# Kernel tuning notes

Hardware: AMD Instinct MI355X
Metric: run time of the kernel (lower is better)

## Reference

```python
import jax, jax.numpy as jnp
import numpy as np

B, S, D_IN = 2, 2048, 1024
H, DA, DH = 16, 64, 64          # num_heads, attention_dim, head_dim (linear_hidden_dim)
EMBED = 1024
KSIZE = 1


def causal_conv1d(x_bsc, w):
    """x_bsc: (B,S,Cin); w: (Cout,Cin,K). Left-pad K-1 -> causal. Returns (B,Cout,S)."""
    k = w.shape[-1]
    x_bcs = jnp.transpose(x_bsc, (0, 2, 1))
    x_bcs = jnp.pad(x_bcs, ((0, 0), (0, 0), (k - 1, 0)))
    return jax.lax.conv_general_dilated(
        x_bcs, w, window_strides=(1,), padding='VALID',
        dimension_numbers=('NCH', 'OIH', 'NCH'))


def setup_inputs() -> dict:
    key = jax.random.key(0)
    ks = jax.random.split(key, 7)
    x = jax.random.normal(ks[0], (B, S, D_IN), dtype=jnp.float32)
    # causal mask: 1 where attended, 0 where masked (masked_fill where ==0)
    attn_mask = jnp.tril(jnp.ones((S, S), dtype=jnp.int32))[None, None]  # (1,1,S,S)
    wq = 0.02 * jax.random.normal(ks[1], (H * DA, D_IN, KSIZE), dtype=jnp.float32)
    wk = 0.02 * jax.random.normal(ks[2], (H * DA, D_IN, KSIZE), dtype=jnp.float32)
    wv = 0.02 * jax.random.normal(ks[3], (H * DH, D_IN, KSIZE), dtype=jnp.float32)
    w_out = 0.02 * jax.random.normal(ks[4], (EMBED, H * DH), dtype=jnp.float32)
    b_out = 0.02 * jax.random.normal(ks[5], (EMBED,), dtype=jnp.float32)
    return {"x": x, "attn_mask": attn_mask, "wq": wq, "wk": wk, "wv": wv,
            "w_out": w_out, "b_out": b_out}


def reference(x, attn_mask, wq, wk, wv, w_out, b_out):
    b, s, _ = x.shape
    scale = DH ** (-0.5)  # NOTE: torch code scales by head_dim, not attention_dim
    q = causal_conv1d(x, wq)  # (B, H*DA, S)
    k = causal_conv1d(x, wk)  # (B, H*DA, S)
    v = causal_conv1d(x, wv)  # (B, H*DH, S)
    q = q.reshape(b, H, DA, s).transpose(0, 1, 3, 2)  # (B,H,S,DA)
    k = k.reshape(b, H, DA, s).transpose(0, 1, 3, 2)
    v = v.reshape(b, H, DH, s).transpose(0, 1, 3, 2)  # (B,H,S,DH)
    scores = scale * jnp.einsum('bhnd,bhmd->bhnm', q, k)
    scores = jnp.where(attn_mask == 0, -jnp.inf, scores)
    probs = jax.nn.softmax(scores, axis=-1)
    context = jnp.einsum('bhnm,bhmd->bhnd', probs, v)  # (B,H,S,DH)
    context = context.transpose(0, 2, 1, 3).reshape(b, s, H * DH)
    return context @ w_out.T + b_out
```

## Files before the change

kernel.cpp:

```cpp
#include <hip/hip_runtime.h>
#include <math.h>


typedef __bf16 bf16;
typedef __bf16 bf16x8 __attribute__((ext_vector_type(8)));
typedef __bf16 bf16x4 __attribute__((ext_vector_type(4)));
typedef float  f32x4  __attribute__((ext_vector_type(4)));

#define MFMA16(a, b, c) __builtin_amdgcn_mfma_f32_16x16x32_bf16((a), (b), (c), 0, 0, 0)

__device__ __forceinline__ void gll16(const void* g, void* l) {
    __builtin_amdgcn_global_load_lds(
        (__attribute__((address_space(1))) unsigned int*)g,
        (__attribute__((address_space(3))) unsigned int*)l, 16, 0, 0);
}

__global__ __launch_bounds__(256) void cvt_all_kernel(
    const float* __restrict__ x,  const float* __restrict__ wq,
    const float* __restrict__ wk, const float* __restrict__ wv,
    const float* __restrict__ wo,
    bf16* __restrict__ xb,  bf16* __restrict__ wqb, bf16* __restrict__ wkb,
    bf16* __restrict__ wvb, bf16* __restrict__ wob)
{
    #pragma unroll
    for (int k = 0; k < 4; k++) {
        const int blk = blockIdx.x * 4 + k;
        const float* src; bf16* dst; int off; float scale = 1.f;
        if (blk < 4096)      { src = x;  dst = xb;  off = blk * 1024; }
        else if (blk < 5120) { src = wq; dst = wqb; off = (blk - 4096) * 1024;
                               scale = 0.18033688011112042f; }
        else if (blk < 6144) { src = wk; dst = wkb; off = (blk - 5120) * 1024; }
        else if (blk < 7168) { src = wv; dst = wvb; off = (blk - 6144) * 1024; }
        else                 { src = wo; dst = wob; off = (blk - 7168) * 1024; }
        const int i = off + threadIdx.x * 4;
        f32x4 v = *(const f32x4*)(src + i);
        bf16x4 o;
        o[0] = (bf16)(v[0] * scale); o[1] = (bf16)(v[1] * scale);
        o[2] = (bf16)(v[2] * scale); o[3] = (bf16)(v[3] * scale);
        *(bf16x4*)(dst + i) = o;
    }
}

__global__ __launch_bounds__(256, 3) void qkv_mfma_kernel(
    const bf16* __restrict__ xb, const bf16* __restrict__ wqb,
    const bf16* __restrict__ wkb, const bf16* __restrict__ wvb,
    bf16* __restrict__ Qb, bf16* __restrict__ Kb, bf16* __restrict__ Vtb)
{
    __shared__ bf16 As[2][128 * 32];
    __shared__ bf16 Bs[2][128 * 32];
    const int lin = blockIdx.x + 32 * blockIdx.y;
    const int xcd = lin & 7, lid = lin >> 3;
    const int rem = xcd * 96 + lid;
    const int mt = rem & 31;
    const int nt = rem >> 5;
    const int which = nt >> 3;
    const bf16* Wm = (which == 0) ? wqb : (which == 1) ? wkb : wvb;

    const int t = threadIdx.x;
    const int w = t >> 6, lane = t & 63, quad = lane >> 4, l16 = lane & 15;
    const int wm = (w >> 1) * 64, wn = (w & 1) * 64;
    const int srow = lane >> 2;
    const int scol = (lane & 3) * 8;

    const bf16* Ab = xb + ((size_t)(mt * 128) + srow) * 1024 + scol;
    const bf16* Bb = Wm + ((size_t)((nt & 7) * 128) + srow) * 1024 + scol;

    f32x4 acc[4][4];
    #pragma unroll
    for (int i = 0; i < 4; i++)
        #pragma unroll
        for (int j = 0; j < 4; j++)
            #pragma unroll
            for (int r = 0; r < 4; r++) acc[i][j][r] = 0.f;

    gll16(Ab + (size_t)(w * 16) * 1024,       As[0] + w * 512);
    gll16(Ab + (size_t)((w + 4) * 16) * 1024, As[0] + (w + 4) * 512);
    gll16(Bb + (size_t)(w * 16) * 1024,       Bs[0] + w * 512);
    gll16(Bb + (size_t)((w + 4) * 16) * 1024, Bs[0] + (w + 4) * 512);

    for (int it = 0; it < 32; it++) {
        const int cur = it & 1, nxt = cur ^ 1;
        __syncthreads();
        if (it < 31) {
            const int kn = it * 32 + 32;
            gll16(Ab + (size_t)(w * 16) * 1024 + kn,       As[nxt] + w * 512);
            gll16(Ab + (size_t)((w + 4) * 16) * 1024 + kn, As[nxt] + (w + 4) * 512);
            gll16(Bb + (size_t)(w * 16) * 1024 + kn,       Bs[nxt] + w * 512);
            gll16(Bb + (size_t)((w + 4) * 16) * 1024 + kn, Bs[nxt] + (w + 4) * 512);
        }
        bf16x8 af[4], bfr[4];
        #pragma unroll
        for (int i = 0; i < 4; i++)
            af[i] = *(const bf16x8*)&As[cur][(wm + i * 16 + l16) * 32 + quad * 8];
        #pragma unroll
        for (int j = 0; j < 4; j++)
            bfr[j] = *(const bf16x8*)&Bs[cur][(wn + j * 16 + l16) * 32 + quad * 8];
        #pragma unroll
        for (int i = 0; i < 4; i++)
            #pragma unroll
            for (int j = 0; j < 4; j++)
                acc[i][j] = MFMA16(af[i], bfr[j], acc[i][j]);
    }

    const int nbase = (nt & 7) * 128 + wn;
    if (which == 2) {
        #pragma unroll
        for (int i = 0; i < 4; i++) {
            const int m0 = mt * 128 + wm + i * 16 + quad * 4;
            const int bb = m0 >> 11, s0 = m0 & 2047;
            #pragma unroll
            for (int j = 0; j < 4; j++) {
                const int n = nbase + j * 16 + l16;
                const int h = n >> 6, d = n & 63;
                bf16x4 pk;
                #pragma unroll
                for (int r = 0; r < 4; r++) pk[r] = (bf16)acc[i][j][r];
                *(bf16x4*)&Vtb[(((size_t)(bb * 16 + h)) * 64 + d) * 2048 + s0] = pk;
            }
        }
    } else {
        bf16* Out = (which == 0) ? Qb : Kb;
        #pragma unroll
        for (int i = 0; i < 4; i++) {
            #pragma unroll
            for (int r = 0; r < 4; r++) {
                const int m = mt * 128 + wm + i * 16 + quad * 4 + r;
                const int bb = m >> 11, s = m & 2047;
                #pragma unroll
                for (int j = 0; j < 4; j++) {
                    const int n = nbase + j * 16 + l16;
                    const int h = n >> 6, d = n & 63;
                    Out[(((size_t)(bb * 16 + h)) * 2048 + s) * 64 + d] =
                        (bf16)acc[i][j][r];
                }
            }
        }
    }
}

__global__ __launch_bounds__(256, 2) void attn_mfma_kernel(
    const bf16* __restrict__ Qb, const bf16* __restrict__ Kb,
    const bf16* __restrict__ Vtb, bf16* __restrict__ ctxb)
{
    __shared__ bf16 Ks[2][128 * 64];
    __shared__ bf16 Vts[2][64 * 128];
    __shared__ bf16 Pl[4][16 * 128];

    const int id = blockIdx.x;
    const int bh = id & 31;
    const int pr = id >> 5;
    const int qa = pr, qb = 31 - pr;
    const int h = bh & 15, b = bh >> 4;
    const int t = threadIdx.x;
    const int w = t >> 6, lane = t & 63, quad = lane >> 4, l16 = lane & 15;

    const size_t hb = (size_t)(b * 16 + h);
    const bf16* Qh = Qb + hb * (2048 * 64);
    const bf16* Kh = Kb + hb * (2048 * 64);
    const bf16* Vh = Vtb + hb * (64 * 2048);

    bf16x8 qf0[2], qf1[2];
    {
        const bf16* Qr0 = Qh + (size_t)(qa * 64 + w * 16 + l16) * 64;
        qf0[0] = *(const bf16x8*)(Qr0 + quad * 8);
        qf0[1] = *(const bf16x8*)(Qr0 + 32 + quad * 8);
        const bf16* Qr1 = Qh + (size_t)(qb * 64 + w * 16 + l16) * 64;
        qf1[0] = *(const bf16x8*)(Qr1 + quad * 8);
        qf1[1] = *(const bf16x8*)(Qr1 + 32 + quad * 8);
    }

    bf16x8 ones;
    #pragma unroll
    for (int i = 0; i < 8; i++) ones[i] = (bf16)1.0f;

    f32x4 o0[4], o1[4], l0, l1;
    #pragma unroll
    for (int r = 0; r < 4; r++) { l0[r] = 0.f; l1[r] = 0.f; }
    #pragma unroll
    for (int dt = 0; dt < 4; dt++)
        #pragma unroll
        for (int r = 0; r < 4; r++) { o0[dt][r] = 0.f; o1[dt][r] = 0.f; }

    const int ksr = lane >> 3, ksc = lane & 7;
    const int vsr = lane >> 4, vsc = lane & 15;

    #define STAGE(ktv, buf)                                                   \
        {                                                                     \
            _Pragma("unroll")                                                 \
            for (int j = 0; j < 4; j++) {                                     \
                const int c = 4 * w + j;                                      \
                const int kr = c * 8 + ksr;                                   \
                gll16(Kh + (size_t)((ktv) * 128 + kr) * 64 +                  \
                          ((ksc ^ (kr & 7)) * 8),                             \
                      Ks[buf] + c * 512);                                     \
                const int vr = c * 4 + vsr;                                   \
                gll16(Vh + (size_t)vr * 2048 + (ktv) * 128 +                  \
                          ((vsc ^ (vr & 15)) * 8),                            \
                      Vts[buf] + c * 512);                                    \
            }                                                                 \
        }

    #define ITER(qt64, ktv, diag, qfv, oacc, lacc, cur)                       \
        {                                                                     \
            f32x4 sacc[8];                                                    \
            __builtin_amdgcn_s_setprio(1);                                    \
            _Pragma("unroll")                                                 \
            for (int tt = 0; tt < 8; tt++) {                                  \
                _Pragma("unroll")                                             \
                for (int r = 0; r < 4; r++) sacc[tt][r] = 0.f;                \
                const int krow = tt * 16 + l16;                               \
                bf16x8 kf0 = *(const bf16x8*)&Ks[cur][krow * 64 +             \
                                 ((quad)     ^ (krow & 7)) * 8];              \
                bf16x8 kf1 = *(const bf16x8*)&Ks[cur][krow * 64 +             \
                                 ((quad + 4) ^ (krow & 7)) * 8];              \
                sacc[tt] = MFMA16(kf0, (qfv)[0], sacc[tt]);                   \
                sacc[tt] = MFMA16(kf1, (qfv)[1], sacc[tt]);                   \
            }                                                                 \
            __builtin_amdgcn_s_setprio(0);                                    \
            const int qrow = (qt64) * 64 + w * 16 + l16;                      \
            _Pragma("unroll")                                                 \
            for (int tt = 0; tt < 8; tt++) {                                  \
                bf16x4 pk;                                                    \
                _Pragma("unroll")                                             \
                for (int r = 0; r < 4; r++) {                                 \
                    float p = __builtin_amdgcn_exp2f(sacc[tt][r]);            \
                    if ((diag) && ((ktv) * 128 + tt * 16 + quad * 4 + r) > qrow) \
                        p = 0.f;                                              \
                    pk[r] = (bf16)p;                                          \
                }                                                             \
                const int cs = (tt * 2 + (quad >> 1)) ^ l16;                  \
                *(bf16x4*)&Pl[w][l16 * 128 + cs * 8 + (quad & 1) * 4] = pk;   \
            }                                                                 \
            bf16x8 ap[4];                                                     \
            __builtin_amdgcn_s_setprio(1);                                    \
            _Pragma("unroll")                                                 \
            for (int u = 0; u < 4; u++) {                                     \
                ap[u] = *(const bf16x8*)&Pl[w][l16 * 128 +                    \
                             ((quad + 4 * u) ^ l16) * 8];                     \
                (lacc) = MFMA16(ap[u], ones, (lacc));                         \
            }                                                                 \
            _Pragma("unroll")                                                 \
            for (int dt = 0; dt < 4; dt++) {                                  \
                const int drow = dt * 16 + l16;                               \
                _Pragma("unroll")                                             \
                for (int u = 0; u < 4; u++) {                                 \
                    bf16x8 bv = *(const bf16x8*)&Vts[cur][drow * 128 +        \
                                     ((4 * u + quad) ^ (drow & 15)) * 8];     \
                    (oacc)[dt] = MFMA16(ap[u], bv, (oacc)[dt]);               \
                }                                                             \
            }                                                                 \
            __builtin_amdgcn_s_setprio(0);                                    \
        }

    const int na = (qa >> 1) + 1;
    STAGE(0, 0);

    for (int v = 0; v < 17; v++) {
        const int cur = v & 1, nxt = cur ^ 1;
        __syncthreads();
        if (v < 16) {
            const int vn = v + 1;
            const int ktn = (vn < na) ? vn : vn - na;
            STAGE(ktn, nxt);
        }
        if (v < na) {
            ITER(qa, v, (v == na - 1), qf0, o0, l0, cur);
        } else {
            const int kt = v - na;
            ITER(qb, kt, (v == 16), qf1, o1, l1, cur);
        }
    }
    #undef STAGE
    #undef ITER

    #pragma unroll
    for (int r = 0; r < 4; r++) {
        const float inv0 = 1.f / l0[r];
        const int s0 = qa * 64 + w * 16 + quad * 4 + r;
        const float inv1 = 1.f / l1[r];
        const int s1 = qb * 64 + w * 16 + quad * 4 + r;
        #pragma unroll
        for (int dt = 0; dt < 4; dt++) {
            ctxb[((size_t)(b * 2048 + s0)) * 1024 + h * 64 + dt * 16 + l16] =
                (bf16)(o0[dt][r] * inv0);
            ctxb[((size_t)(b * 2048 + s1)) * 1024 + h * 64 + dt * 16 + l16] =
                (bf16)(o1[dt][r] * inv1);
        }
    }
}

__global__ __launch_bounds__(256, 2) void oproj_mfma_kernel(
    const bf16* __restrict__ ctxb, const bf16* __restrict__ wob,
    const float* __restrict__ b_out, float* __restrict__ out)
{
    __shared__ bf16 As[2][64 * 32];
    __shared__ bf16 Bs[2][128 * 32];
    const int mt = blockIdx.x;
    const int nt = blockIdx.y;
    const int t = threadIdx.x;
    const int w = t >> 6, lane = t & 63, quad = lane >> 4, l16 = lane & 15;
    const int srow = lane >> 2;
    const int scol = (lane & 3) * 8;

    const bf16* Ab = ctxb + (size_t)(mt * 64 + srow) * 1024 + scol;
    const bf16* Bb = wob + (size_t)(nt * 128 + srow) * 1024 + scol;

    const int wrow = (w >> 1) * 32;
    const int wcol = (w & 1) * 64;

    f32x4 acc[2][4];
    #pragma unroll
    for (int i = 0; i < 2; i++)
        #pragma unroll
        for (int j = 0; j < 4; j++)
            #pragma unroll
            for (int r = 0; r < 4; r++) acc[i][j][r] = 0.f;

    gll16(Ab + (size_t)(w * 16) * 1024,       As[0] + w * 512);
    gll16(Bb + (size_t)(w * 16) * 1024,       Bs[0] + w * 512);
    gll16(Bb + (size_t)((w + 4) * 16) * 1024, Bs[0] + (w + 4) * 512);

    for (int it = 0; it < 32; it++) {
        const int cur = it & 1, nxt = cur ^ 1;
        __syncthreads();
        if (it < 31) {
            const int kn = it * 32 + 32;
            gll16(Ab + (size_t)(w * 16) * 1024 + kn,       As[nxt] + w * 512);
            gll16(Bb + (size_t)(w * 16) * 1024 + kn,       Bs[nxt] + w * 512);
            gll16(Bb + (size_t)((w + 4) * 16) * 1024 + kn, Bs[nxt] + (w + 4) * 512);
        }
        bf16x8 af0 = *(const bf16x8*)&As[cur][(wrow + l16) * 32 + quad * 8];
        bf16x8 af1 = *(const bf16x8*)&As[cur][(wrow + 16 + l16) * 32 + quad * 8];
        #pragma unroll
        for (int j = 0; j < 4; j++) {
            bf16x8 bv = *(const bf16x8*)&Bs[cur][(wcol + j * 16 + l16) * 32 + quad * 8];
            acc[0][j] = MFMA16(af0, bv, acc[0][j]);
            acc[1][j] = MFMA16(af1, bv, acc[1][j]);
        }
    }

    #pragma unroll
    for (int i = 0; i < 2; i++)
        #pragma unroll
        for (int j = 0; j < 4; j++)
            #pragma unroll
            for (int r = 0; r < 4; r++) {
                const int m = mt * 64 + wrow + i * 16 + quad * 4 + r;
                const int n = nt * 128 + wcol + j * 16 + l16;
                out[(size_t)m * 1024 + n] = acc[i][j][r] + b_out[n];
            }
}

extern "C" void kernel_launch(void* const* d_in, const int* in_sizes, int n_in,
                              void* d_out, int out_size, void* d_ws, size_t ws_size,
                              hipStream_t stream)
{
    const float* x     = (const float*)d_in[0];
    const float* wq    = (const float*)d_in[2];
    const float* wk    = (const float*)d_in[3];
    const float* wv    = (const float*)d_in[4];
    const float* w_out = (const float*)d_in[5];
    const float* b_out = (const float*)d_in[6];
    float* out = (float*)d_out;

    char* ws = (char*)d_ws;
    bf16* xb   = (bf16*)(ws);
    bf16* wqb  = (bf16*)(ws + (8u  << 20));
    bf16* wkb  = (bf16*)(ws + (10u << 20));
    bf16* wvb  = (bf16*)(ws + (12u << 20));
    bf16* wob  = (bf16*)(ws + (14u << 20));
    bf16* Qb   = (bf16*)(ws + (16u << 20));
    bf16* Kb   = (bf16*)(ws + (24u << 20));
    bf16* Vtb  = (bf16*)(ws + (32u << 20));
    bf16* ctxb = (bf16*)(ws + (40u << 20));

    cvt_all_kernel<<<2048, 256, 0, stream>>>(x, wq, wk, wv, w_out,
                                             xb, wqb, wkb, wvb, wob);
    qkv_mfma_kernel<<<dim3(32, 24), 256, 0, stream>>>(xb, wqb, wkb, wvb, Qb, Kb, Vtb);
    attn_mfma_kernel<<<512, 256, 0, stream>>>(Qb, Kb, Vtb, ctxb);
    oproj_mfma_kernel<<<dim3(64, 8), 256, 0, stream>>>(ctxb, wob, b_out, out);
}
```

Measured before the change: 187.1 us.

## Rewrite QKV projection GEMM with 256x256 tiles, 8 waves, swizzled LDS and fine-grained pipeline

Replaces the 128x128x32 double-buffered QKV GEMM with a 256x256 tile computed by 512-thread blocks (8 waves), using K-steps of 64 and XOR-swizzled LDS layouts to avoid bank conflicts. The main loop interleaves global-to-LDS loads of half-tiles with MFMA phases under explicit barriers, vmcnt waits and setprio, so loads overlap with compute. This raises arithmetic intensity and cuts global traffic per FLOP, but the grid shrinks to 192 blocks, which may underfill the device, and register and LDS pressure rise.

```diff
diff --git a/kernel.cpp b/kernel.cpp
--- a/kernel.cpp
+++ b/kernel.cpp
@@ -41,96 +41,187 @@
     }
 }
 
-__global__ __launch_bounds__(256, 3) void qkv_mfma_kernel(
+__global__ __launch_bounds__(512, 2) void qkv_mfma_kernel(
     const bf16* __restrict__ xb, const bf16* __restrict__ wqb,
     const bf16* __restrict__ wkb, const bf16* __restrict__ wvb,
     bf16* __restrict__ Qb, bf16* __restrict__ Kb, bf16* __restrict__ Vtb)
 {
-    __shared__ bf16 As[2][128 * 32];
-    __shared__ bf16 Bs[2][128 * 32];
-    const int lin = blockIdx.x + 32 * blockIdx.y;
-    const int xcd = lin & 7, lid = lin >> 3;
-    const int rem = xcd * 96 + lid;
-    const int mt = rem & 31;
-    const int nt = rem >> 5;
-    const int which = nt >> 3;
+    __shared__ bf16 Asm[2][2][128 * 64];
+    __shared__ bf16 Bsm[2][2][128 * 64];
+
+    const int lin = blockIdx.x;
+    const int rem = (lin & 7) * 24 + (lin >> 3);
+    const int mt = rem / 12;
+    const int nt = rem % 12;
+    const int which = nt >> 2;
     const bf16* Wm = (which == 0) ? wqb : (which == 1) ? wkb : wvb;
 
     const int t = threadIdx.x;
     const int w = t >> 6, lane = t & 63, quad = lane >> 4, l16 = lane & 15;
-    const int wm = (w >> 1) * 64, wn = (w & 1) * 64;
-    const int srow = lane >> 2;
-    const int scol = (lane & 3) * 8;
-
-    const bf16* Ab = xb + ((size_t)(mt * 128) + srow) * 1024 + scol;
-    const bf16* Bb = Wm + ((size_t)((nt & 7) * 128) + srow) * 1024 + scol;
-
-    f32x4 acc[4][4];
-    #pragma unroll
-    for (int i = 0; i < 4; i++)
+    const int ha  = w >> 2;
+    const int hbi = (w & 3) >> 1;
+    const int br0 = (w & 1) * 64;
+
+    const int srA = w * 8 + (lane >> 3);
+    const int scg = ((lane & 7) ^ (lane >> 3)) * 8;
+
+    const int MT0 = mt * 256;
+    const int NT0 = (nt & 3) * 256;
+
+    const int xr = l16 & 7;
+    const int cg0 = ((quad)     ^ xr) * 8;
+    const int cg1 = ((quad + 4) ^ xr) * 8;
+
+    f32x4 acc[8][4];
+    #pragma unroll
+    for (int i = 0; i < 8; i++)
         #pragma unroll
         for (int j = 0; j < 4; j++)
             #pragma unroll
             for (int r = 0; r < 4; r++) acc[i][j][r] = 0.f;
 
-    gll16(Ab + (size_t)(w * 16) * 1024,       As[0] + w * 512);
-    gll16(Ab + (size_t)((w + 4) * 16) * 1024, As[0] + (w + 4) * 512);
-    gll16(Bb + (size_t)(w * 16) * 1024,       Bs[0] + w * 512);
-    gll16(Bb + (size_t)((w + 4) * 16) * 1024, Bs[0] + (w + 4) * 512);
-
-    for (int it = 0; it < 32; it++) {
-        const int cur = it & 1, nxt = cur ^ 1;
-        __syncthreads();
-        if (it < 31) {
-            const int kn = it * 32 + 32;
-            gll16(Ab + (size_t)(w * 16) * 1024 + kn,       As[nxt] + w * 512);
-            gll16(Ab + (size_t)((w + 4) * 16) * 1024 + kn, As[nxt] + (w + 4) * 512);
-            gll16(Bb + (size_t)(w * 16) * 1024 + kn,       Bs[nxt] + w * 512);
-            gll16(Bb + (size_t)((w + 4) * 16) * 1024 + kn, Bs[nxt] + (w + 4) * 512);
-        }
-        bf16x8 af[4], bfr[4];
-        #pragma unroll
-        for (int i = 0; i < 4; i++)
-            af[i] = *(const bf16x8*)&As[cur][(wm + i * 16 + l16) * 32 + quad * 8];
-        #pragma unroll
-        for (int j = 0; j < 4; j++)
-            bfr[j] = *(const bf16x8*)&Bs[cur][(wn + j * 16 + l16) * 32 + quad * 8];
-        #pragma unroll
-        for (int i = 0; i < 4; i++)
-            #pragma unroll
-            for (int j = 0; j < 4; j++)
-                acc[i][j] = MFMA16(af[i], bfr[j], acc[i][j]);
-    }
-
-    const int nbase = (nt & 7) * 128 + wn;
+    bf16x8 af0[4][2], af1[4][2], bf0[2][2], bf1[2][2];
+
+#define STG(gb, R0, kb, dst)                                                  \
+    gll16((gb) + (size_t)((R0) + srA) * 1024 + (kb) + scg, (dst) + w * 512);  \
+    gll16((gb) + (size_t)((R0) + 64 + srA) * 1024 + (kb) + scg,               \
+          (dst) + 4096 + w * 512);
+
+#define LDA(dst, DB, IB)                                                      \
+    _Pragma("unroll")                                                         \
+    for (int ii = 0; ii < 4; ii++) {                                          \
+        const int ro = ((IB) + ii) * 16 + l16;                                \
+        dst[ii][0] = *(const bf16x8*)&Asm[DB][ha][ro * 64 + cg0];             \
+        dst[ii][1] = *(const bf16x8*)&Asm[DB][ha][ro * 64 + cg1];             \
+    }
+
+#define LDB(dst, DB, JB)                                                      \
+    _Pragma("unroll")                                                         \
+    for (int jj = 0; jj < 2; jj++) {                                          \
+        const int ro = br0 + ((JB) + jj) * 16 + l16;                          \
+        dst[jj][0] = *(const bf16x8*)&Bsm[DB][hbi][ro * 64 + cg0];            \
+        dst[jj][1] = *(const bf16x8*)&Bsm[DB][hbi][ro * 64 + cg1];            \
+    }
+
+#define MM(afv, IB, bfv, JB)                                                  \
+    __builtin_amdgcn_s_setprio(1);                                            \
+    _Pragma("unroll")                                                         \
+    for (int ii = 0; ii < 4; ii++)                                            \
+        _Pragma("unroll")                                                     \
+        for (int jj = 0; jj < 2; jj++) {                                      \
+            acc[(IB) + ii][(JB) + jj] =                                       \
+                MFMA16(afv[ii][0], bfv[jj][0], acc[(IB) + ii][(JB) + jj]);    \
+            acc[(IB) + ii][(JB) + jj] =                                       \
+                MFMA16(afv[ii][1], bfv[jj][1], acc[(IB) + ii][(JB) + jj]);    \
+        }                                                                     \
+    __builtin_amdgcn_s_setprio(0);
+
+#define BARR __builtin_amdgcn_s_barrier()
+#define LG0  asm volatile("s_waitcnt lgkmcnt(0)" ::: "memory")
+#define VM4  asm volatile("s_waitcnt vmcnt(4)" ::: "memory")
+#define VM0  asm volatile("s_waitcnt vmcnt(0)" ::: "memory")
+
+    STG(xb, MT0,       0, &Asm[0][0][0]);
+    STG(xb, MT0 + 128, 0, &Asm[0][1][0]);
+    STG(Wm, NT0,       0, &Bsm[0][0][0]);
+    STG(Wm, NT0 + 128, 0, &Bsm[0][1][0]);
+    STG(Wm, NT0,      64, &Bsm[1][0][0]);
+    STG(Wm, NT0 + 128,64, &Bsm[1][1][0]);
+    VM4;
+    BARR;
+
+    for (int tt = 0; tt < 8; tt++) {
+        const int kB = tt * 128 + 64;
+        const int kC = tt * 128 + 128;
+        const int kD = tt * 128 + 192;
+        const bool more = (tt < 7);
+
+        LDA(af0, 0, 0); LDB(bf0, 0, 0);
+        STG(xb, MT0,       kB, &Asm[1][0][0]);
+        BARR; LG0;
+        MM(af0, 0, bf0, 0);
+        BARR;
+
+        LDA(af1, 0, 4); LDB(bf1, 0, 2);
+        STG(xb, MT0 + 128, kB, &Asm[1][1][0]);
+        BARR; LG0;
+        MM(af1, 4, bf0, 0);
+        BARR;
+
+        if (more) { STG(Wm, NT0,       kC, &Bsm[0][0][0]); }
+        BARR;
+        MM(af0, 0, bf1, 2);
+        BARR;
+
+        if (more) { STG(Wm, NT0 + 128, kC, &Bsm[0][1][0]); }
+        BARR;
+        MM(af1, 4, bf1, 2);
+        if (more) { VM4; } else { VM0; }
+        BARR;
+
+        LDA(af0, 1, 0); LDB(bf0, 1, 0);
+        if (more) { STG(xb, MT0,       kC, &Asm[0][0][0]); }
+        BARR; LG0;
+        MM(af0, 0, bf0, 0);
+        BARR;
+
+        LDA(af1, 1, 4); LDB(bf1, 1, 2);
+        if (more) { STG(xb, MT0 + 128, kC, &Asm[0][1][0]); }
+        BARR; LG0;
+        MM(af1, 4, bf0, 0);
+        BARR;
+
+        if (more) { STG(Wm, NT0,       kD, &Bsm[1][0][0]); }
+        BARR;
+        MM(af0, 0, bf1, 2);
+        BARR;
+
+        if (more) { STG(Wm, NT0 + 128, kD, &Bsm[1][1][0]); }
+        BARR;
+        MM(af1, 4, bf1, 2);
+        VM4;
+        BARR;
+    }
+
+#undef STG
+#undef LDA
+#undef LDB
+#undef MM
+#undef BARR
+#undef LG0
+#undef VM4
+#undef VM0
+
+    const int wrowg = MT0 + ha * 128;
+    const int ncol  = NT0 + (w & 3) * 64;
     if (which == 2) {
         #pragma unroll
-        for (int i = 0; i < 4; i++) {
-            const int m0 = mt * 128 + wm + i * 16 + quad * 4;
+        for (int i = 0; i < 8; i++) {
+            const int m0 = wrowg + i * 16 + quad * 4;
             const int bb = m0 >> 11, s0 = m0 & 2047;
             #pragma unroll
             for (int j = 0; j < 4; j++) {
-                const int n = nbase + j * 16 + l16;
-                const int h = n >> 6, d = n & 63;
+                const int n = ncol + j * 16 + l16;
+                const int hh = n >> 6, dd = n & 63;
                 bf16x4 pk;
                 #pragma unroll
                 for (int r = 0; r < 4; r++) pk[r] = (bf16)acc[i][j][r];
-                *(bf16x4*)&Vtb[(((size_t)(bb * 16 + h)) * 64 + d) * 2048 + s0] = pk;
+                *(bf16x4*)&Vtb[(((size_t)(bb * 16 + hh)) * 64 + dd) * 2048 + s0] = pk;
             }
         }
     } else {
         bf16* Out = (which == 0) ? Qb : Kb;
         #pragma unroll
-        for (int i = 0; i < 4; i++) {
+        for (int i = 0; i < 8; i++) {
             #pragma unroll
             for (int r = 0; r < 4; r++) {
-                const int m = mt * 128 + wm + i * 16 + quad * 4 + r;
+                const int m = wrowg + i * 16 + quad * 4 + r;
                 const int bb = m >> 11, s = m & 2047;
                 #pragma unroll
                 for (int j = 0; j < 4; j++) {
-                    const int n = nbase + j * 16 + l16;
-                    const int h = n >> 6, d = n & 63;
-                    Out[(((size_t)(bb * 16 + h)) * 2048 + s) * 64 + d] =
+                    const int n = ncol + j * 16 + l16;
+                    const int hh = n >> 6, dd = n & 63;
+                    Out[(((size_t)(bb * 16 + hh)) * 2048 + s) * 64 + dd] =
                         (bf16)acc[i][j][r];
                 }
             }
@@ -376,7 +467,7 @@
 
     cvt_all_kernel<<<2048, 256, 0, stream>>>(x, wq, wk, wv, w_out,
                                              xb, wqb, wkb, wvb, wob);
-    qkv_mfma_kernel<<<dim3(32, 24), 256, 0, stream>>>(xb, wqb, wkb, wvb, Qb, Kb, Vtb);
+    qkv_mfma_kernel<<<192, 512, 0, stream>>>(xb, wqb, wkb, wvb, Qb, Kb, Vtb);
     attn_mfma_kernel<<<512, 256, 0, stream>>>(Qb, Kb, Vtb, ctxb);
     oproj_mfma_kernel<<<dim3(64, 8), 256, 0, stream>>>(ctxb, wob, b_out, out);
 }
```

Result: slower. 197.7 us (+5.7%).

## Double K-tile depth in output projection GEMM with XOR-swizzled LDS

Applied to the files above, without the earlier changes.

The output projection GEMM now stages 64-wide K slices instead of 32, halving the number of barrier-separated iterations. It also XOR-swizzles the LDS column groups so fragment reads avoid bank conflicts, and raises the occupancy hint to 3 blocks per CU. The cost is twice the shared memory per block and more live fragment registers, which could cap occupancy. This kernel is only one stage of the full pipeline.

```diff
diff --git a/kernel.cpp b/kernel.cpp
--- a/kernel.cpp
+++ b/kernel.cpp
@@ -289,25 +289,25 @@
     }
 }
 
-__global__ __launch_bounds__(256, 2) void oproj_mfma_kernel(
+__global__ __launch_bounds__(256, 3) void oproj_mfma_kernel(
     const bf16* __restrict__ ctxb, const bf16* __restrict__ wob,
     const float* __restrict__ b_out, float* __restrict__ out)
 {
-    __shared__ bf16 As[2][64 * 32];
-    __shared__ bf16 Bs[2][128 * 32];
+    __shared__ bf16 As[2][64 * 64];
+    __shared__ bf16 Bs[2][128 * 64];
     const int mt = blockIdx.x;
     const int nt = blockIdx.y;
     const int t = threadIdx.x;
     const int w = t >> 6, lane = t & 63, quad = lane >> 4, l16 = lane & 15;
-    const int srow = lane >> 2;
-    const int scol = (lane & 3) * 8;
-
-    const bf16* Ab = ctxb + (size_t)(mt * 64 + srow) * 1024 + scol;
-    const bf16* Bb = wob + (size_t)(nt * 128 + srow) * 1024 + scol;
+    const int srow8 = lane >> 3;
+    const int scg = ((lane & 7) ^ srow8) * 8;
 
     const int wrow = (w >> 1) * 32;
     const int wcol = (w & 1) * 64;
 
+    const bf16* Ab = ctxb + (size_t)(mt * 64) * 1024;
+    const bf16* Bb = wob + (size_t)(nt * 128) * 1024;
+
     f32x4 acc[2][4];
     #pragma unroll
     for (int i = 0; i < 2; i++)
@@ -316,28 +316,48 @@
             #pragma unroll
             for (int r = 0; r < 4; r++) acc[i][j][r] = 0.f;
 
-    gll16(Ab + (size_t)(w * 16) * 1024,       As[0] + w * 512);
-    gll16(Bb + (size_t)(w * 16) * 1024,       Bs[0] + w * 512);
-    gll16(Bb + (size_t)((w + 4) * 16) * 1024, Bs[0] + (w + 4) * 512);
-
-    for (int it = 0; it < 32; it++) {
+    #define OSTG(buf, kk)                                                     \
+        {                                                                     \
+            gll16(Ab + (size_t)(w * 8 + srow8) * 1024 + (kk) + scg,           \
+                  As[buf] + w * 512);                                         \
+            gll16(Ab + (size_t)((w + 4) * 8 + srow8) * 1024 + (kk) + scg,     \
+                  As[buf] + (w + 4) * 512);                                   \
+            _Pragma("unroll")                                                 \
+            for (int c = 0; c < 4; c++) {                                     \
+                const int ch = w + 4 * c;                                     \
+                gll16(Bb + (size_t)(ch * 8 + srow8) * 1024 + (kk) + scg,      \
+                      Bs[buf] + ch * 512);                                    \
+            }                                                                 \
+        }
+
+    OSTG(0, 0);
+
+    for (int it = 0; it < 16; it++) {
         const int cur = it & 1, nxt = cur ^ 1;
         __syncthreads();
-        if (it < 31) {
-            const int kn = it * 32 + 32;
-            gll16(Ab + (size_t)(w * 16) * 1024 + kn,       As[nxt] + w * 512);
-            gll16(Bb + (size_t)(w * 16) * 1024 + kn,       Bs[nxt] + w * 512);
-            gll16(Bb + (size_t)((w + 4) * 16) * 1024 + kn, Bs[nxt] + (w + 4) * 512);
-        }
-        bf16x8 af0 = *(const bf16x8*)&As[cur][(wrow + l16) * 32 + quad * 8];
-        bf16x8 af1 = *(const bf16x8*)&As[cur][(wrow + 16 + l16) * 32 + quad * 8];
+        if (it < 15) { OSTG(nxt, it * 64 + 64); }
+        bf16x8 af[2][2], bfv[4][2];
+        #pragma unroll
+        for (int i = 0; i < 2; i++) {
+            const int ro = wrow + i * 16 + l16;
+            af[i][0] = *(const bf16x8*)&As[cur][ro * 64 + ((quad)     ^ (ro & 7)) * 8];
+            af[i][1] = *(const bf16x8*)&As[cur][ro * 64 + ((quad + 4) ^ (ro & 7)) * 8];
+        }
         #pragma unroll
         for (int j = 0; j < 4; j++) {
-            bf16x8 bv = *(const bf16x8*)&Bs[cur][(wcol + j * 16 + l16) * 32 + quad * 8];
-            acc[0][j] = MFMA16(af0, bv, acc[0][j]);
-            acc[1][j] = MFMA16(af1, bv, acc[1][j]);
-        }
-    }
+            const int ro = wcol + j * 16 + l16;
+            bfv[j][0] = *(const bf16x8*)&Bs[cur][ro * 64 + ((quad)     ^ (ro & 7)) * 8];
+            bfv[j][1] = *(const bf16x8*)&Bs[cur][ro * 64 + ((quad + 4) ^ (ro & 7)) * 8];
+        }
+        #pragma unroll
+        for (int i = 0; i < 2; i++)
+            #pragma unroll
+            for (int j = 0; j < 4; j++) {
+                acc[i][j] = MFMA16(af[i][0], bfv[j][0], acc[i][j]);
+                acc[i][j] = MFMA16(af[i][1], bfv[j][1], acc[i][j]);
+            }
+    }
+    #undef OSTG
 
     #pragma unroll
     for (int i = 0; i < 2; i++)
```

New measurement: 179.3 us. 1.04x faster.
